# Kernel tuning notes

Measured on AMD Instinct MI355X. Metric: run time of the kernel, lower is better.

## Reference

```python
import jax, jax.numpy as jnp
import numpy as np

N = 100000
E = 1600000
F_IN = 64
HEADS = 4
HID = 16
NUM_CLASSES = 2
NEG_SLOPE = 0.2


def setup_inputs() -> dict:
    key = jax.random.key(0)
    ks = jax.random.split(key, 12)
    inputs = jax.random.normal(ks[0], (N, F_IN), dtype=jnp.float32)
    edge_index = jax.random.randint(ks[1], (2, E), 0, N, dtype=jnp.int64)
    edge_attr = jax.random.uniform(ks[2], (E,), dtype=jnp.float32)
    # layer 1 params (GATConv: lin has no bias; final bias of size heads*out)
    s1 = 1.0 / np.sqrt(F_IN)
    W1 = jax.random.uniform(ks[3], (F_IN, HEADS * HID), jnp.float32, -s1, s1)
    att_src1 = jax.random.uniform(ks[4], (HEADS, HID), jnp.float32, -s1, s1)
    att_dst1 = jax.random.uniform(ks[5], (HEADS, HID), jnp.float32, -s1, s1)
    b1 = jnp.zeros((HEADS * HID,), jnp.float32)
    # layer 2 params (heads=1)
    s2 = 1.0 / np.sqrt(HEADS * HID)
    W2 = jax.random.uniform(ks[6], (HEADS * HID, NUM_CLASSES), jnp.float32, -s2, s2)
    att_src2 = jax.random.uniform(ks[7], (1, NUM_CLASSES), jnp.float32, -s2, s2)
    att_dst2 = jax.random.uniform(ks[8], (1, NUM_CLASSES), jnp.float32, -s2, s2)
    b2 = jnp.zeros((NUM_CLASSES,), jnp.float32)
    return {"inputs": inputs, "edge_index": edge_index, "edge_attr": edge_attr,
            "W1": W1, "att_src1": att_src1, "att_dst1": att_dst1, "b1": b1,
            "W2": W2, "att_src2": att_src2, "att_dst2": att_dst2, "b2": b2}


def _add_self_loops(edge_index):
    loop = jnp.arange(N, dtype=edge_index.dtype)
    src = jnp.concatenate([edge_index[0], loop])
    dst = jnp.concatenate([edge_index[1], loop])
    return src, dst


def _gat_layer(x, src, dst, W, a_src, a_dst, bias, heads, out_ch):
    h = (x @ W).reshape(N, heads, out_ch)              # [N,H,C]
    alpha_s = jnp.einsum('nhc,hc->nh', h, a_src)        # [N,H]
    alpha_d = jnp.einsum('nhc,hc->nh', h, a_dst)        # [N,H]
    e = jax.nn.leaky_relu(alpha_s[src] + alpha_d[dst], NEG_SLOPE)  # [E,H]
    # softmax over incoming edges per destination node
    m = jax.ops.segment_max(e, dst, num_segments=N)
    m = jnp.where(jnp.isfinite(m), m, 0.0)
    ex = jnp.exp(e - m[dst])
    denom = jax.ops.segment_sum(ex, dst, num_segments=N)
    alpha = ex / (denom[dst] + 1e-16)                   # [E,H]
    msg = h[src] * alpha[:, :, None]                    # [E,H,C]
    out = jax.ops.segment_sum(msg, dst, num_segments=N) # [N,H,C]
    return out.reshape(N, heads * out_ch) + bias


def reference(inputs, edge_index, edge_attr,
              W1, att_src1, att_dst1, b1,
              W2, att_src2, att_dst2, b2):
    # edge_attr is ignored by GATConv when edge_dim is None (as in the source)
    src, dst = _add_self_loops(edge_index)
    x = _gat_layer(inputs, src, dst, W1, att_src1, att_dst1, b1, HEADS, HID)
    x = jax.nn.relu(x)
    x = _gat_layer(x, src, dst, W2, att_src2, att_dst2, b2, 1, NUM_CLASSES)
    return x
```

## Files before the change

### kernel.cpp

```cpp
#include <hip/hip_runtime.h>
#include <hip/hip_fp16.h>

#define N_NODES 100000
#define NE      1600000
#define ETOT    (NE + N_NODES)
#define F1      64
#define NEG     0.2f
#define CAP     48

#define PBITS   8
#define PSZ     (1 << PBITS)
#define NPART   ((N_NODES + PSZ - 1) / PSZ)
#define N_PAD   (NPART * PSZ)
#define PCAP    5120
#define K2_EPT  8
#define K2_BLK  1024
#define K2_TILE (K2_BLK * K2_EPT)

#define GT      128

static inline int cdiv(int a, int b) { return (a + b - 1) / b; }

__global__ __launch_bounds__(K2_BLK) void partition(
        const int* __restrict__ src, const int* __restrict__ dst,
        int* __restrict__ pcur, int* __restrict__ pairs) {
    __shared__ int hist[NPART];
    __shared__ int base[NPART];
    int t = threadIdx.x;
    for (int i = t; i < NPART; i += K2_BLK) hist[i] = 0;
    __syncthreads();

    int e0 = blockIdx.x * K2_TILE + t;
    int b8[K2_EPT], pos8[K2_EPT], pk8[K2_EPT];
#pragma unroll
    for (int i = 0; i < K2_EPT; ++i) {
        int e = e0 + i * K2_BLK;
        b8[i] = -1;
        if (e < ETOT) {
            int s, d;
            if (e < NE) { s = src[e]; d = dst[e]; } else { s = d = e - NE; }
            int b = d >> PBITS;
            b8[i] = b;
            pk8[i] = ((d & (PSZ - 1)) << 17) | s;
            pos8[i] = atomicAdd(&hist[b], 1);
        }
    }
    __syncthreads();
    for (int i = t; i < NPART; i += K2_BLK)
        base[i] = atomicAdd(&pcur[i], hist[i]);
    __syncthreads();
#pragma unroll
    for (int i = 0; i < K2_EPT; ++i) {
        if (b8[i] >= 0) {
            int idx = base[b8[i]] + pos8[i];
            if (idx < PCAP) pairs[b8[i] * PCAP + idx] = pk8[i];
        }
    }
}

__global__ __launch_bounds__(256) void fine_scatter(
        const int* __restrict__ pcur, const int* __restrict__ pairs,
        int* __restrict__ cnt, int* __restrict__ esrc) {
    __shared__ int lcnt[PSZ];
    __shared__ int lsrc[PSZ * CAP];
    int p = blockIdx.x, t = threadIdx.x;
    for (int i = t; i < PSZ; i += 256) lcnt[i] = 0;
    __syncthreads();

    int np = pcur[p];
    np = np < PCAP ? np : PCAP;
    const int* pp = pairs + p * PCAP;
    for (int i = t; i < np; i += 256) {
        int v = pp[i];
        int ld = v >> 17;
        int s = v & 0x1FFFF;
        int pos = atomicAdd(&lcnt[ld], 1);
        if (pos < CAP) lsrc[ld * CAP + pos] = s;
    }
    __syncthreads();

    int nb = p << PBITS;
    for (int i = t; i < PSZ; i += 256)
        if (nb + i < N_NODES) cnt[nb + i] = lcnt[i];
    int* eo = esrc + (size_t)nb * CAP;
    for (int i = t; i < PSZ * CAP; i += 256) eo[i] = lsrc[i];
}

__global__ __launch_bounds__(256) void gemm_fused(
        const float* __restrict__ x, const float* __restrict__ W,
        const float* __restrict__ a_src, const float* __restrict__ a_dst,
        __half* __restrict__ h1h, float* __restrict__ as1, float* __restrict__ ad1) {
    __shared__ float sW[64 * 64];
    __shared__ float sXT[64 * 128];
    int t = threadIdx.x;
    int n0 = blockIdx.x * GT;

    for (int i = t; i < 1024; i += 256) ((float4*)sW)[i] = ((const float4*)W)[i];

    for (int i = t; i < 2048; i += 256) {
        int n = i >> 4, kq = i & 15;
        float4 v = make_float4(0.f, 0.f, 0.f, 0.f);
        if (n0 + n < N_NODES) v = ((const float4*)(x + (size_t)(n0 + n) * 64))[kq];
        int k0 = kq * 4, n4 = n >> 2, nl = n & 3;
        sXT[(k0 + 0) * 128 + (((n4 ^ (k0 + 0)) & 31) << 2) + nl] = v.x;
        sXT[(k0 + 1) * 128 + (((n4 ^ (k0 + 1)) & 31) << 2) + nl] = v.y;
        sXT[(k0 + 2) * 128 + (((n4 ^ (k0 + 2)) & 31) << 2) + nl] = v.z;
        sXT[(k0 + 3) * 128 + (((n4 ^ (k0 + 3)) & 31) << 2) + nl] = v.w;
    }
    __syncthreads();

    int jo = t & 7, nq = t >> 3;
    int jo8 = jo * 8;
    float acc[4][8];
#pragma unroll
    for (int m = 0; m < 4; ++m)
#pragma unroll
        for (int c = 0; c < 8; ++c) acc[m][c] = 0.f;

#pragma unroll 4
    for (int k = 0; k < 64; ++k) {
        const float4 xv = *(const float4*)&sXT[k * 128 + (((nq ^ k) & 31) << 2)];
        const float4 w0 = *(const float4*)&sW[k * 64 + jo8];
        const float4 w1 = *(const float4*)&sW[k * 64 + jo8 + 4];
        float xm[4] = {xv.x, xv.y, xv.z, xv.w};
        float wv[8] = {w0.x, w0.y, w0.z, w0.w, w1.x, w1.y, w1.z, w1.w};
#pragma unroll
        for (int m = 0; m < 4; ++m)
#pragma unroll
            for (int c = 0; c < 8; ++c)
                acc[m][c] = fmaf(xm[m], wv[c], acc[m][c]);
    }

    float av[8], dv[8];
#pragma unroll
    for (int c = 0; c < 8; ++c) { av[c] = a_src[jo8 + c]; dv[c] = a_dst[jo8 + c]; }

#pragma unroll
    for (int m = 0; m < 4; ++m) {
        int n = n0 + nq * 4 + m;
        if (n < N_NODES) {
            __half hb[8];
#pragma unroll
            for (int c = 0; c < 8; ++c) hb[c] = __float2half(acc[m][c]);
            *(uint4*)(h1h + (size_t)n * 64 + jo8) = *(const uint4*)hb;
        }
        float ps = 0.f, pd = 0.f;
#pragma unroll
        for (int c = 0; c < 8; ++c) {
            ps = fmaf(acc[m][c], av[c], ps);
            pd = fmaf(acc[m][c], dv[c], pd);
        }
        ps += __shfl_xor(ps, 1, 64);
        pd += __shfl_xor(pd, 1, 64);
        if ((jo & 1) == 0 && n < N_NODES) {
            as1[n * 4 + (jo >> 1)] = ps;
            ad1[n * 4 + (jo >> 1)] = pd;
        }
    }
}

template <int NIT>
__device__ __forceinline__ void rounds(const int* __restrict__ bucket, int deg,
                                       int grp, int sub, int h, float ad,
                                       const __half* __restrict__ h1h,
                                       const float* __restrict__ as1,
                                       float num[8], float& den) {
    int s[NIT];
#pragma unroll
    for (int r = 0; r < NIT; ++r) {
        int ei = r * 8 + grp;
        s[r] = bucket[ei < deg ? ei : 0];
    }
    float a[NIT];
    uint4 g[NIT];
#pragma unroll
    for (int r = 0; r < NIT; ++r) {
        a[r] = as1[s[r] * 4 + h];
        g[r] = *(const uint4*)(h1h + (size_t)s[r] * 64 + sub * 8);
    }
#pragma unroll
    for (int r = 0; r < NIT; ++r) {
        bool act = (r * 8 + grp) < deg;
        float v = a[r] + ad;
        v = v > 0.f ? v : NEG * v;
        float ex = act ? __expf(v) : 0.f;
        const __half2* hp = (const __half2*)&g[r];
#pragma unroll
        for (int q = 0; q < 4; ++q) {
            float2 f = __half22float2(hp[q]);
            num[q * 2 + 0] = fmaf(ex, f.x, num[q * 2 + 0]);
            num[q * 2 + 1] = fmaf(ex, f.y, num[q * 2 + 1]);
        }
        den += ex;
    }
}

__global__ void aggr1(const int* __restrict__ cnt, const int* __restrict__ esrc,
                      const __half* __restrict__ h1h, const float* __restrict__ as1,
                      const float* __restrict__ ad1, const float* __restrict__ b1,
                      const float* __restrict__ W2, const float* __restrict__ a_src2,
                      const float* __restrict__ a_dst2, float4* __restrict__ pack2) {
    int gid = blockIdx.x * blockDim.x + threadIdx.x;
    int w = gid >> 6;
    if (w >= N_NODES) return;
    int lane = threadIdx.x & 63;
    int grp = lane >> 3, sub = lane & 7, h = sub >> 1;
    int deg = cnt[w];
    deg = deg < CAP ? deg : CAP;
    const int* bucket = esrc + (size_t)w * CAP;
    float ad = ad1[w * 4 + h];
    float num[8];
#pragma unroll
    for (int c = 0; c < 8; ++c) num[c] = 0.f;
    float den = 0.f;

    int nit = (deg + 7) >> 3;
    if (nit == 1)      rounds<1>(bucket, deg, grp, sub, h, ad, h1h, as1, num, den);
    else if (nit == 2) rounds<2>(bucket, deg, grp, sub, h, ad, h1h, as1, num, den);
    else if (nit == 3) rounds<3>(bucket, deg, grp, sub, h, ad, h1h, as1, num, den);
    else               rounds<6>(bucket, deg, grp, sub, h, ad, h1h, as1, num, den);

#pragma unroll
    for (int d = 8; d < 64; d <<= 1) {
#pragma unroll
        for (int c = 0; c < 8; ++c) num[c] += __shfl_xor(num[c], d, 64);
        den += __shfl_xor(den, d, 64);
    }
    if (grp == 0) {
        float inv = 1.f / (den + 1e-16f);
        const float4 ba = ((const float4*)b1)[sub * 2];
        const float4 bb = ((const float4*)b1)[sub * 2 + 1];
        float o[8];
        o[0] = fmaf(num[0], inv, ba.x); o[1] = fmaf(num[1], inv, ba.y);
        o[2] = fmaf(num[2], inv, ba.z); o[3] = fmaf(num[3], inv, ba.w);
        o[4] = fmaf(num[4], inv, bb.x); o[5] = fmaf(num[5], inv, bb.y);
        o[6] = fmaf(num[6], inv, bb.z); o[7] = fmaf(num[7], inv, bb.w);
        const float4* w2p = (const float4*)(W2 + sub * 16);
        float4 w2v0 = w2p[0], w2v1 = w2p[1], w2v2 = w2p[2], w2v3 = w2p[3];
        float wtmp[16] = {w2v0.x, w2v0.y, w2v0.z, w2v0.w,
                          w2v1.x, w2v1.y, w2v1.z, w2v1.w,
                          w2v2.x, w2v2.y, w2v2.z, w2v2.w,
                          w2v3.x, w2v3.y, w2v3.z, w2v3.w};
        float p0 = 0.f, p1 = 0.f;
#pragma unroll
        for (int c = 0; c < 8; ++c) {
            float r = fmaxf(o[c], 0.f);
            p0 = fmaf(r, wtmp[c * 2 + 0], p0);
            p1 = fmaf(r, wtmp[c * 2 + 1], p1);
        }
        p0 += __shfl_xor(p0, 1, 64); p1 += __shfl_xor(p1, 1, 64);
        p0 += __shfl_xor(p0, 2, 64); p1 += __shfl_xor(p1, 2, 64);
        p0 += __shfl_xor(p0, 4, 64); p1 += __shfl_xor(p1, 4, 64);
        if (sub == 0) {
            float4 pk;
            pk.x = p0;
            pk.y = p1;
            pk.z = p0 * a_src2[0] + p1 * a_src2[1];
            pk.w = p0 * a_dst2[0] + p1 * a_dst2[1];
            pack2[w] = pk;
        }
    }
}

__global__ void aggr2(const int* __restrict__ cnt, const int* __restrict__ esrc,
                      const float4* __restrict__ pack2, const float* __restrict__ b2,
                      float* __restrict__ out) {
    int gid = blockIdx.x * blockDim.x + threadIdx.x;
    int w = gid >> 6;
    if (w >= N_NODES) return;
    int lane = threadIdx.x & 63;
    int deg = cnt[w];
    deg = deg < CAP ? deg : CAP;
    const int* bucket = esrc + (size_t)w * CAP;
    float adv = pack2[w].w;
    bool act = lane < deg;
    int s = bucket[act ? lane : 0];
    float4 ps = pack2[s];
    float v = ps.z + adv;
    v = v > 0.f ? v : NEG * v;
    float ex = act ? __expf(v) : 0.f;
    float n0 = ex * ps.x, n1 = ex * ps.y, den = ex;
#pragma unroll
    for (int d = 1; d < 64; d <<= 1) {
        n0  += __shfl_xor(n0, d, 64);
        n1  += __shfl_xor(n1, d, 64);
        den += __shfl_xor(den, d, 64);
    }
    if (lane == 0) {
        float inv = 1.f / (den + 1e-16f);
        float2 o;
        o.x = fmaf(n0, inv, b2[0]);
        o.y = fmaf(n1, inv, b2[1]);
        *(float2*)(out + w * 2) = o;
    }
}

extern "C" void kernel_launch(void* const* d_in, const int* in_sizes, int n_in,
                              void* d_out, int out_size, void* d_ws, size_t ws_size,
                              hipStream_t stream) {
    const float* x        = (const float*)d_in[0];
    const int*   ei       = (const int*)d_in[1];
    const float* W1       = (const float*)d_in[3];
    const float* att_src1 = (const float*)d_in[4];
    const float* att_dst1 = (const float*)d_in[5];
    const float* b1       = (const float*)d_in[6];
    const float* W2       = (const float*)d_in[7];
    const float* att_src2 = (const float*)d_in[8];
    const float* att_dst2 = (const float*)d_in[9];
    const float* b2       = (const float*)d_in[10];

    const int* src = ei;
    const int* dst = ei + NE;
    float* out = (float*)d_out;

    char* p = (char*)d_ws;
    int* pcur     = (int*)p;     p += sizeof(int) * 512;
    int* cnt      = (int*)p;     p += sizeof(int) * N_NODES;
    int* esrc     = (int*)p;     p += sizeof(int) * (size_t)N_PAD * CAP;
    __half* h1h   = (__half*)p;  p += sizeof(__half) * (size_t)N_NODES * F1;
    float* as1    = (float*)p;   p += sizeof(float) * N_NODES * 4;
    float* ad1    = (float*)p;   p += sizeof(float) * N_NODES * 4;
    float4* pack2 = (float4*)p;  p += sizeof(float4) * N_NODES;
    int* pairs    = (int*)p;     p += sizeof(int) * (size_t)NPART * PCAP;

    const int B = 256;

    hipMemsetAsync(pcur, 0, sizeof(int) * 512, stream);
    partition<<<cdiv(ETOT, K2_TILE), K2_BLK, 0, stream>>>(src, dst, pcur, pairs);
    fine_scatter<<<NPART, 256, 0, stream>>>(pcur, pairs, cnt, esrc);
    gemm_fused<<<cdiv(N_NODES, GT), 256, 0, stream>>>(x, W1, att_src1, att_dst1,
                                                      h1h, as1, ad1);
    aggr1<<<cdiv(N_NODES * 64, B), B, 0, stream>>>(cnt, esrc, h1h, as1, ad1, b1,
                                                   W2, att_src2, att_dst2, pack2);
    aggr2<<<cdiv(N_NODES * 64, B), B, 0, stream>>>(cnt, esrc, pack2, b2, out);
}
```

Baseline: 210.2 us.

## Merge edge partition and node GEMM into one interleaved kernel launch

```diff
diff --git a/kernel.cpp b/kernel.cpp
--- a/kernel.cpp
+++ b/kernel.cpp
@@ -14,46 +14,127 @@
 #define N_PAD   (NPART * PSZ)
 #define PCAP    5120
 #define K2_EPT  8
-#define K2_BLK  1024
+#define K2_BLK  256
 #define K2_TILE (K2_BLK * K2_EPT)
+#define NPB     ((ETOT + K2_TILE - 1) / K2_TILE)
 
 #define GT      128
+#define NGB     ((N_NODES + GT - 1) / GT)
 
 static inline int cdiv(int a, int b) { return (a + b - 1) / b; }
 
-__global__ __launch_bounds__(K2_BLK) void partition(
+__global__ __launch_bounds__(256) void part_gemm(
         const int* __restrict__ src, const int* __restrict__ dst,
-        int* __restrict__ pcur, int* __restrict__ pairs) {
-    __shared__ int hist[NPART];
-    __shared__ int base[NPART];
+        int* __restrict__ pcur, int* __restrict__ pairs,
+        const float* __restrict__ x, const float* __restrict__ W,
+        const float* __restrict__ a_src, const float* __restrict__ a_dst,
+        __half* __restrict__ h1h, float* __restrict__ as1, float* __restrict__ ad1) {
+    __shared__ union {
+        struct { int hist[NPART]; int base[NPART]; } p;
+        struct { float sW[64 * 64]; float sXT[64 * 128]; } g;
+    } u;
     int t = threadIdx.x;
-    for (int i = t; i < NPART; i += K2_BLK) hist[i] = 0;
+
+    if ((blockIdx.x & 1) == 0) {
+        int pb = blockIdx.x >> 1;
+        if (pb >= NPB) return;
+        for (int i = t; i < NPART; i += K2_BLK) u.p.hist[i] = 0;
+        __syncthreads();
+
+        int e0 = pb * K2_TILE + t;
+        int b8[K2_EPT], pos8[K2_EPT], pk8[K2_EPT];
+#pragma unroll
+        for (int i = 0; i < K2_EPT; ++i) {
+            int e = e0 + i * K2_BLK;
+            b8[i] = -1;
+            if (e < ETOT) {
+                int s, d;
+                if (e < NE) { s = src[e]; d = dst[e]; } else { s = d = e - NE; }
+                int b = d >> PBITS;
+                b8[i] = b;
+                pk8[i] = ((d & (PSZ - 1)) << 17) | s;
+                pos8[i] = atomicAdd(&u.p.hist[b], 1);
+            }
+        }
+        __syncthreads();
+        for (int i = t; i < NPART; i += K2_BLK)
+            u.p.base[i] = atomicAdd(&pcur[i], u.p.hist[i]);
+        __syncthreads();
+#pragma unroll
+        for (int i = 0; i < K2_EPT; ++i) {
+            if (b8[i] >= 0) {
+                int idx = u.p.base[b8[i]] + pos8[i];
+                if (idx < PCAP) pairs[b8[i] * PCAP + idx] = pk8[i];
+            }
+        }
+        return;
+    }
+
+    int gb = blockIdx.x >> 1;
+    if (gb >= NGB) return;
+    int n0 = gb * GT;
+
+    for (int i = t; i < 1024; i += 256)
+        ((float4*)u.g.sW)[i] = ((const float4*)W)[i];
+
+    for (int i = t; i < 2048; i += 256) {
+        int n = i >> 4, kq = i & 15;
+        float4 v = make_float4(0.f, 0.f, 0.f, 0.f);
+        if (n0 + n < N_NODES) v = ((const float4*)(x + (size_t)(n0 + n) * 64))[kq];
+        int k0 = kq * 4, n4 = n >> 2, nl = n & 3;
+        u.g.sXT[(k0 + 0) * 128 + (((n4 ^ (k0 + 0)) & 31) << 2) + nl] = v.x;
+        u.g.sXT[(k0 + 1) * 128 + (((n4 ^ (k0 + 1)) & 31) << 2) + nl] = v.y;
+        u.g.sXT[(k0 + 2) * 128 + (((n4 ^ (k0 + 2)) & 31) << 2) + nl] = v.z;
+        u.g.sXT[(k0 + 3) * 128 + (((n4 ^ (k0 + 3)) & 31) << 2) + nl] = v.w;
+    }
     __syncthreads();
 
-    int e0 = blockIdx.x * K2_TILE + t;
-    int b8[K2_EPT], pos8[K2_EPT], pk8[K2_EPT];
-#pragma unroll
-    for (int i = 0; i < K2_EPT; ++i) {
-        int e = e0 + i * K2_BLK;
-        b8[i] = -1;
-        if (e < ETOT) {
-            int s, d;
-            if (e < NE) { s = src[e]; d = dst[e]; } else { s = d = e - NE; }
-            int b = d >> PBITS;
-            b8[i] = b;
-            pk8[i] = ((d & (PSZ - 1)) << 17) | s;
-            pos8[i] = atomicAdd(&hist[b], 1);
-        }
-    }
-    __syncthreads();
-    for (int i = t; i < NPART; i += K2_BLK)
-        base[i] = atomicAdd(&pcur[i], hist[i]);
-    __syncthreads();
-#pragma unroll
-    for (int i = 0; i < K2_EPT; ++i) {
-        if (b8[i] >= 0) {
-            int idx = base[b8[i]] + pos8[i];
-            if (idx < PCAP) pairs[b8[i] * PCAP + idx] = pk8[i];
+    int jo = t & 7, nq = t >> 3;
+    int jo8 = jo * 8;
+    float acc[4][8];
+#pragma unroll
+    for (int m = 0; m < 4; ++m)
+#pragma unroll
+        for (int c = 0; c < 8; ++c) acc[m][c] = 0.f;
+
+#pragma unroll 4
+    for (int k = 0; k < 64; ++k) {
+        const float4 xv = *(const float4*)&u.g.sXT[k * 128 + (((nq ^ k) & 31) << 2)];
+        const float4 w0 = *(const float4*)&u.g.sW[k * 64 + jo8];
+        const float4 w1 = *(const float4*)&u.g.sW[k * 64 + jo8 + 4];
+        float xm[4] = {xv.x, xv.y, xv.z, xv.w};
+        float wv[8] = {w0.x, w0.y, w0.z, w0.w, w1.x, w1.y, w1.z, w1.w};
+#pragma unroll
+        for (int m = 0; m < 4; ++m)
+#pragma unroll
+            for (int c = 0; c < 8; ++c)
+                acc[m][c] = fmaf(xm[m], wv[c], acc[m][c]);
+    }
+
+    float av[8], dv[8];
+#pragma unroll
+    for (int c = 0; c < 8; ++c) { av[c] = a_src[jo8 + c]; dv[c] = a_dst[jo8 + c]; }
+
+#pragma unroll
+    for (int m = 0; m < 4; ++m) {
+        int n = n0 + nq * 4 + m;
+        if (n < N_NODES) {
+            __half hb[8];
+#pragma unroll
+            for (int c = 0; c < 8; ++c) hb[c] = __float2half(acc[m][c]);
+            *(uint4*)(h1h + (size_t)n * 64 + jo8) = *(const uint4*)hb;
+        }
+        float ps = 0.f, pd = 0.f;
+#pragma unroll
+        for (int c = 0; c < 8; ++c) {
+            ps = fmaf(acc[m][c], av[c], ps);
+            pd = fmaf(acc[m][c], dv[c], pd);
+        }
+        ps += __shfl_xor(ps, 1, 64);
+        pd += __shfl_xor(pd, 1, 64);
+        if ((jo & 1) == 0 && n < N_NODES) {
+            as1[n * 4 + (jo >> 1)] = ps;
+            ad1[n * 4 + (jo >> 1)] = pd;
         }
     }
 }
@@ -84,79 +165,6 @@
         if (nb + i < N_NODES) cnt[nb + i] = lcnt[i];
     int* eo = esrc + (size_t)nb * CAP;
     for (int i = t; i < PSZ * CAP; i += 256) eo[i] = lsrc[i];
-}
-
-__global__ __launch_bounds__(256) void gemm_fused(
-        const float* __restrict__ x, const float* __restrict__ W,
-        const float* __restrict__ a_src, const float* __restrict__ a_dst,
-        __half* __restrict__ h1h, float* __restrict__ as1, float* __restrict__ ad1) {
-    __shared__ float sW[64 * 64];
-    __shared__ float sXT[64 * 128];
-    int t = threadIdx.x;
-    int n0 = blockIdx.x * GT;
-
-    for (int i = t; i < 1024; i += 256) ((float4*)sW)[i] = ((const float4*)W)[i];
-
-    for (int i = t; i < 2048; i += 256) {
-        int n = i >> 4, kq = i & 15;
-        float4 v = make_float4(0.f, 0.f, 0.f, 0.f);
-        if (n0 + n < N_NODES) v = ((const float4*)(x + (size_t)(n0 + n) * 64))[kq];
-        int k0 = kq * 4, n4 = n >> 2, nl = n & 3;
-        sXT[(k0 + 0) * 128 + (((n4 ^ (k0 + 0)) & 31) << 2) + nl] = v.x;
-        sXT[(k0 + 1) * 128 + (((n4 ^ (k0 + 1)) & 31) << 2) + nl] = v.y;
-        sXT[(k0 + 2) * 128 + (((n4 ^ (k0 + 2)) & 31) << 2) + nl] = v.z;
-        sXT[(k0 + 3) * 128 + (((n4 ^ (k0 + 3)) & 31) << 2) + nl] = v.w;
-    }
-    __syncthreads();
-
-    int jo = t & 7, nq = t >> 3;
-    int jo8 = jo * 8;
-    float acc[4][8];
-#pragma unroll
-    for (int m = 0; m < 4; ++m)
-#pragma unroll
-        for (int c = 0; c < 8; ++c) acc[m][c] = 0.f;
-
-#pragma unroll 4
-    for (int k = 0; k < 64; ++k) {
-        const float4 xv = *(const float4*)&sXT[k * 128 + (((nq ^ k) & 31) << 2)];
-        const float4 w0 = *(const float4*)&sW[k * 64 + jo8];
-        const float4 w1 = *(const float4*)&sW[k * 64 + jo8 + 4];
-        float xm[4] = {xv.x, xv.y, xv.z, xv.w};
-        float wv[8] = {w0.x, w0.y, w0.z, w0.w, w1.x, w1.y, w1.z, w1.w};
-#pragma unroll
-        for (int m = 0; m < 4; ++m)
-#pragma unroll
-            for (int c = 0; c < 8; ++c)
-                acc[m][c] = fmaf(xm[m], wv[c], acc[m][c]);
-    }
-
-    float av[8], dv[8];
-#pragma unroll
-    for (int c = 0; c < 8; ++c) { av[c] = a_src[jo8 + c]; dv[c] = a_dst[jo8 + c]; }
-
-#pragma unroll
-    for (int m = 0; m < 4; ++m) {
-        int n = n0 + nq * 4 + m;
-        if (n < N_NODES) {
-            __half hb[8];
-#pragma unroll
-            for (int c = 0; c < 8; ++c) hb[c] = __float2half(acc[m][c]);
-            *(uint4*)(h1h + (size_t)n * 64 + jo8) = *(const uint4*)hb;
-        }
-        float ps = 0.f, pd = 0.f;
-#pragma unroll
-        for (int c = 0; c < 8; ++c) {
-            ps = fmaf(acc[m][c], av[c], ps);
-            pd = fmaf(acc[m][c], dv[c], pd);
-        }
-        ps += __shfl_xor(ps, 1, 64);
-        pd += __shfl_xor(pd, 1, 64);
-        if ((jo & 1) == 0 && n < N_NODES) {
-            as1[n * 4 + (jo >> 1)] = ps;
-            ad1[n * 4 + (jo >> 1)] = pd;
-        }
-    }
 }
 
 template <int NIT>
@@ -326,10 +334,9 @@
     const int B = 256;
 
     hipMemsetAsync(pcur, 0, sizeof(int) * 512, stream);
-    partition<<<cdiv(ETOT, K2_TILE), K2_BLK, 0, stream>>>(src, dst, pcur, pairs);
+    part_gemm<<<2 * (NPB > NGB ? NPB : NGB), 256, 0, stream>>>(
+        src, dst, pcur, pairs, x, W1, att_src1, att_dst1, h1h, as1, ad1);
     fine_scatter<<<NPART, 256, 0, stream>>>(pcur, pairs, cnt, esrc);
-    gemm_fused<<<cdiv(N_NODES, GT), 256, 0, stream>>>(x, W1, att_src1, att_dst1,
-                                                      h1h, as1, ad1);
     aggr1<<<cdiv(N_NODES * 64, B), B, 0, stream>>>(cnt, esrc, h1h, as1, ad1, b1,
                                                    W2, att_src2, att_dst2, pack2);
     aggr2<<<cdiv(N_NODES * 64, B), B, 0, stream>>>(cnt, esrc, pack2, b2, out);
```

New measurement: 215.5 us. 1.03x slower.
